# Optimization experiments

Measured on AMD Instinct MI355X. Metric: run time of the kernel, lower is better.

The kernel has to match this reference:

```python
import jax, jax.numpy as jnp
import numpy as np

NUM_USERS = 50000
NUM_ITEMS = 20000
N_NODES = NUM_USERS + NUM_ITEMS
D = 128
CONTENT_DIM = 512
BATCH = 8192
N_EDGES = 500000
NEG_SLOPE = 0.2  # GATConv leaky_relu slope


def setup_inputs() -> dict:
    key = jax.random.key(0)
    ks = jax.random.split(key, 16)
    return {
        "user_ids": jax.random.randint(ks[0], (BATCH,), 0, NUM_USERS),
        "item_ids": jax.random.randint(ks[1], (BATCH,), 0, NUM_ITEMS),
        "content_features": jax.random.normal(ks[2], (BATCH, CONTENT_DIM), jnp.float32),
        "edge_index": jax.random.randint(ks[3], (2, N_EDGES), 0, N_NODES),
        "user_emb_w": jax.random.normal(ks[4], (NUM_USERS, D), jnp.float32) * 0.05,
        "item_emb_w": jax.random.normal(ks[5], (NUM_ITEMS, D), jnp.float32) * 0.05,
        "content_proj_w": jax.random.normal(ks[6], (D, CONTENT_DIM), jnp.float32) * 0.04,
        "content_proj_b": jnp.zeros((D,), jnp.float32),
        "conv1_lin_w": jax.random.normal(ks[7], (2 * D, 2 * D), jnp.float32) * 0.06,
        "conv1_att_src": jax.random.normal(ks[8], (2, D), jnp.float32) * 0.1,
        "conv1_att_dst": jax.random.normal(ks[9], (2, D), jnp.float32) * 0.1,
        "conv1_bias": jnp.zeros((2 * D,), jnp.float32),
        "conv2_lin_w": jax.random.normal(ks[10], (D, 2 * D), jnp.float32) * 0.06,
        "conv2_att_src": jax.random.normal(ks[11], (1, D), jnp.float32) * 0.1,
        "conv2_att_dst": jax.random.normal(ks[12], (1, D), jnp.float32) * 0.1,
        "conv2_bias": jnp.zeros((D,), jnp.float32),
        "pred_w1": jax.random.normal(ks[13], (D, 3 * D), jnp.float32) * 0.05,
        "pred_b1": jnp.zeros((D,), jnp.float32),
        "pred_w2": jax.random.normal(ks[14], (1, D), jnp.float32) * 0.09,
        "pred_b2": jnp.zeros((1,), jnp.float32),
    }


def gat_conv(x, src, dst, lin_w, att_src, att_dst, bias, heads, out_ch):
    # PyG GATConv (shared lin for src/dst, concat=True, add_self_loops handled outside)
    n = x.shape[0]
    h = (x @ lin_w.T).reshape(n, heads, out_ch)          # [N,H,C]
    a_src = jnp.sum(h * att_src, axis=-1)                # [N,H]
    a_dst = jnp.sum(h * att_dst, axis=-1)                # [N,H]
    alpha = jax.nn.leaky_relu(a_src[src] + a_dst[dst], NEG_SLOPE)  # [E,H]
    # softmax over incoming edges of each destination node
    amax = jax.ops.segment_max(alpha, dst, num_segments=n)
    ex = jnp.exp(alpha - amax[dst])
    denom = jax.ops.segment_sum(ex, dst, num_segments=n)
    w = ex / denom[dst]                                  # [E,H]
    out = jax.ops.segment_sum(h[src] * w[:, :, None], dst, num_segments=n)
    return out.reshape(n, heads * out_ch) + bias


def _forward(user_ids, item_ids, edge_index, content_features, user_emb_w, item_emb_w,
             content_proj_w, content_proj_b, conv1_lin_w, conv1_att_src, conv1_att_dst,
             conv1_bias, conv2_lin_w, conv2_att_src, conv2_att_dst, conv2_bias,
             pred_w1, pred_b1, pred_w2, pred_b2):
    u_emb = user_emb_w[user_ids]                         # [B,D]
    i_emb = item_emb_w[item_ids]                         # [B,D]
    c_emb = content_features @ content_proj_w.T + content_proj_b  # [B,D]
    # scatter-init sparse node features (only batch nodes are nonzero, as in source)
    x = jnp.zeros((N_NODES, 2 * D), jnp.float32)
    x = x.at[user_ids].set(jnp.concatenate([u_emb, jnp.zeros_like(c_emb)], axis=1))
    x = x.at[NUM_USERS + item_ids].set(jnp.concatenate([i_emb, c_emb], axis=1))
    # add self loops (fill_value irrelevant: edge_weight unused by GATConv)
    loops = jnp.arange(N_NODES, dtype=edge_index.dtype)
    src = jnp.concatenate([edge_index[0], loops])
    dst = jnp.concatenate([edge_index[1], loops])
    x = jax.nn.elu(gat_conv(x, src, dst, conv1_lin_w, conv1_att_src, conv1_att_dst, conv1_bias, 2, D))
    # dropout inactive (eval mode)
    x = gat_conv(x, src, dst, conv2_lin_w, conv2_att_src, conv2_att_dst, conv2_bias, 1, D)
    combined = jnp.concatenate([u_emb, x[NUM_USERS + item_ids], x[user_ids]], axis=1)  # [B,3D]
    h = jax.nn.relu(combined @ pred_w1.T + pred_b1)
    return (h @ pred_w2.T + pred_b2).squeeze(-1)         # [B]


def reference(user_ids, item_ids, content_features, edge_index, user_emb_w, item_emb_w,
              content_proj_w, content_proj_b, conv1_lin_w, conv1_att_src, conv1_att_dst,
              conv1_bias, conv2_lin_w, conv2_att_src, conv2_att_dst, conv2_bias,
              pred_w1, pred_b1, pred_w2, pred_b2):
    return _forward(user_ids, item_ids, edge_index, content_features, user_emb_w, item_emb_w,
                    content_proj_w, content_proj_b, conv1_lin_w, conv1_att_src, conv1_att_dst,
                    conv1_bias, conv2_lin_w, conv2_att_src, conv2_att_dst, conv2_bias,
                    pred_w1, pred_b1, pred_w2, pred_b2)
```

## Files before the change

### kernel.cpp

```cpp
#include <hip/hip_runtime.h>
#include <hip/hip_bf16.h>

#define NU 50000
#define NI 20000
#define NN 70000
#define DD 128
#define BB 8192
#define EE 500000
#define ET 570000
#define NTASK 16384

__device__ __forceinline__ float lrelu(float x) { return x > 0.f ? x : 0.2f * x; }

typedef __attribute__((ext_vector_type(8))) short bf16x8;
typedef __attribute__((ext_vector_type(8))) unsigned short u16x8;
typedef __attribute__((ext_vector_type(4))) float f32x4;

__device__ __forceinline__ unsigned short f2bf_rne(float f) {
  unsigned int u = __builtin_bit_cast(unsigned int, f);
  u += 0x7FFFu + ((u >> 16) & 1u);
  return (unsigned short)(u >> 16);
}
__device__ __forceinline__ float bf2f(unsigned short h) {
  unsigned int u = ((unsigned int)h) << 16;
  return __builtin_bit_cast(float, u);
}

template <int GATHER>
__global__ __launch_bounds__(256) void gemm_mfma(
    const float* __restrict__ A,
    const unsigned short* __restrict__ Bh, const unsigned short* __restrict__ Bl,
    const float* __restrict__ bias, float* __restrict__ C, int ldc,
    int M, int N, int K, int act,
    const int* __restrict__ idx0, const int* __restrict__ idx1,
    const int* __restrict__ mapv,
    const float* __restrict__ gA0, const float* __restrict__ gA1) {
  __shared__ __align__(16) unsigned short sAh[8][64][8];
  __shared__ __align__(16) unsigned short sAl[8][64][8];
  __shared__ __align__(16) unsigned short sBh[8][64][8];
  __shared__ __align__(16) unsigned short sBl[8][64][8];
  int tid = threadIdx.x;
  int bm = blockIdx.x * 64, bn = blockIdx.y * 64;
  int lane = tid & 63, w = tid >> 6;
  int wr = (w >> 1) * 32, wc = (w & 1) * 32;
  int fr = lane & 15, fk = lane >> 4;
  f32x4 acc[2][2] = {};

  for (int k0 = 0; k0 < K; k0 += 64) {
    __syncthreads();
#pragma unroll
    for (int t = 0; t < 2; t++) {
      int f = tid + t * 256;
      int row = f >> 3, kb = f & 7;
      int kg = k0 + kb * 8;
      const float* ap;
      if (GATHER == 1) {
        int sec = kg >> 7;
        int kc = kg & 127;
        int r = bm + row;
        if (sec == 0)      ap = &gA0[(size_t)idx0[r] * 128 + kc];
        else if (sec == 1) ap = &gA1[(size_t)mapv[NU + idx1[r]] * 128 + kc];
        else               ap = &gA1[(size_t)mapv[idx0[r]] * 128 + kc];
      } else if (GATHER == 2) {
        ap = &gA0[(size_t)idx0[bm + row] * K + kg];
      } else {
        ap = &A[(size_t)(bm + row) * K + kg];
      }
      float4 v0 = *reinterpret_cast<const float4*>(ap);
      float4 v1 = *reinterpret_cast<const float4*>(ap + 4);
      float vv[8] = {v0.x, v0.y, v0.z, v0.w, v1.x, v1.y, v1.z, v1.w};
      u16x8 hv, lv;
#pragma unroll
      for (int j = 0; j < 8; j++) {
        unsigned short hh = f2bf_rne(vv[j]);
        hv[j] = hh;
        lv[j] = (unsigned short)(__builtin_bit_cast(unsigned int, vv[j] - bf2f(hh)) >> 16);
      }
      *reinterpret_cast<u16x8*>(&sAh[kb][row][0]) = hv;
      *reinterpret_cast<u16x8*>(&sAl[kb][row][0]) = lv;
    }
#pragma unroll
    for (int t = 0; t < 2; t++) {
      int f = tid + t * 256;
      int row = f >> 3, kb = f & 7;
      int kg = k0 + kb * 8;
      *reinterpret_cast<u16x8*>(&sBh[kb][row][0]) =
          *reinterpret_cast<const u16x8*>(&Bh[(size_t)(bn + row) * K + kg]);
      *reinterpret_cast<u16x8*>(&sBl[kb][row][0]) =
          *reinterpret_cast<const u16x8*>(&Bl[(size_t)(bn + row) * K + kg]);
    }
    __syncthreads();
#pragma unroll
    for (int s = 0; s < 2; s++) {
      int kb = s * 4 + fk;
      bf16x8 ah0 = *reinterpret_cast<const bf16x8*>(&sAh[kb][wr + fr][0]);
      bf16x8 ah1 = *reinterpret_cast<const bf16x8*>(&sAh[kb][wr + 16 + fr][0]);
      bf16x8 al0 = *reinterpret_cast<const bf16x8*>(&sAl[kb][wr + fr][0]);
      bf16x8 al1 = *reinterpret_cast<const bf16x8*>(&sAl[kb][wr + 16 + fr][0]);
      bf16x8 bh0 = *reinterpret_cast<const bf16x8*>(&sBh[kb][wc + fr][0]);
      bf16x8 bh1 = *reinterpret_cast<const bf16x8*>(&sBh[kb][wc + 16 + fr][0]);
      bf16x8 bl0 = *reinterpret_cast<const bf16x8*>(&sBl[kb][wc + fr][0]);
      bf16x8 bl1 = *reinterpret_cast<const bf16x8*>(&sBl[kb][wc + 16 + fr][0]);
      acc[0][0] = __builtin_amdgcn_mfma_f32_16x16x32_bf16(al0, bh0, acc[0][0], 0, 0, 0);
      acc[0][0] = __builtin_amdgcn_mfma_f32_16x16x32_bf16(ah0, bl0, acc[0][0], 0, 0, 0);
      acc[0][0] = __builtin_amdgcn_mfma_f32_16x16x32_bf16(ah0, bh0, acc[0][0], 0, 0, 0);
      acc[0][1] = __builtin_amdgcn_mfma_f32_16x16x32_bf16(al0, bh1, acc[0][1], 0, 0, 0);
      acc[0][1] = __builtin_amdgcn_mfma_f32_16x16x32_bf16(ah0, bl1, acc[0][1], 0, 0, 0);
      acc[0][1] = __builtin_amdgcn_mfma_f32_16x16x32_bf16(ah0, bh1, acc[0][1], 0, 0, 0);
      acc[1][0] = __builtin_amdgcn_mfma_f32_16x16x32_bf16(al1, bh0, acc[1][0], 0, 0, 0);
      acc[1][0] = __builtin_amdgcn_mfma_f32_16x16x32_bf16(ah1, bl0, acc[1][0], 0, 0, 0);
      acc[1][0] = __builtin_amdgcn_mfma_f32_16x16x32_bf16(ah1, bh0, acc[1][0], 0, 0, 0);
      acc[1][1] = __builtin_amdgcn_mfma_f32_16x16x32_bf16(al1, bh1, acc[1][1], 0, 0, 0);
      acc[1][1] = __builtin_amdgcn_mfma_f32_16x16x32_bf16(ah1, bl1, acc[1][1], 0, 0, 0);
      acc[1][1] = __builtin_amdgcn_mfma_f32_16x16x32_bf16(ah1, bh1, acc[1][1], 0, 0, 0);
    }
  }
#pragma unroll
  for (int j = 0; j < 2; j++) {
    int col = bn + wc + j * 16 + fr;
    float bj = bias ? bias[col] : 0.f;
#pragma unroll
    for (int i = 0; i < 2; i++) {
#pragma unroll
      for (int r = 0; r < 4; r++) {
        int row = bm + wr + i * 16 + fk * 4 + r;
        float v = acc[i][j][r] + bj;
        if (act == 1) v = fmaxf(v, 0.f);
        C[(size_t)row * ldc + col] = v;
      }
    }
  }
}

#define EB 2227
#define SPLB 832
#define XAB 4096
__global__ __launch_bounds__(256) void setup_kernel(
    const int* __restrict__ ei, const int* __restrict__ uid, const int* __restrict__ iid,
    int* __restrict__ deg, int* __restrict__ winner,
    const float* __restrict__ wc, unsigned short* wch, unsigned short* wcl,
    const float* __restrict__ w1, unsigned short* w1h, unsigned short* w1l,
    const float* __restrict__ w2, unsigned short* w2h, unsigned short* w2l,
    const float* __restrict__ pw1, unsigned short* p1h, unsigned short* p1l,
    const float* __restrict__ uemb, const float* __restrict__ iemb,
    float* __restrict__ Xa, int* __restrict__ map) {
  int bid = blockIdx.x, tid = threadIdx.x;
  if (bid < EB) {
    int e = bid * 256 + tid;
    if (e < BB) atomicMax(&winner[iid[e]], e);
    if (e >= ET) return;
    int dst = (e < EE) ? ei[EE + e] : (e - EE);
    atomicAdd(&deg[dst], 1);
    return;
  }
  if (bid < EB + SPLB) {
    int i = (bid - EB) * 256 + tid;
    const float* w; unsigned short* h; unsigned short* l; int idx;
    if (i < 65536) { w = wc; h = wch; l = wcl; idx = i; }
    else if (i < 131072) { w = w1; h = w1h; l = w1l; idx = i - 65536; }
    else if (i < 163840) { w = w2; h = w2h; l = w2l; idx = i - 131072; }
    else { w = pw1; h = p1h; l = p1l; idx = i - 163840; }
    float f = w[idx];
    unsigned short hh = f2bf_rne(f);
    h[idx] = hh;
    l[idx] = (unsigned short)(__builtin_bit_cast(unsigned int, f - bf2f(hh)) >> 16);
    return;
  }
  int t = (bid - EB - SPLB) * 4 + (tid >> 6);
  int lane = tid & 63;
  int c4 = lane * 4;
  if (t < BB) {
    int u = uid[t];
    float4 v = make_float4(0.f, 0.f, 0.f, 0.f);
    if (c4 < DD) v = *reinterpret_cast<const float4*>(&uemb[(size_t)u * DD + c4]);
    *reinterpret_cast<float4*>(&Xa[(size_t)t * 256 + c4]) = v;
    if (lane == 0) map[u] = t;
  } else {
    int it = iid[t - BB];
    if (c4 < DD) {
      float4 v = *reinterpret_cast<const float4*>(&iemb[(size_t)it * DD + c4]);
      *reinterpret_cast<float4*>(&Xa[(size_t)t * 256 + c4]) = v;
    }
    if (lane == 0) map[NU + it] = t;
  }
}

__global__ void rowstart_kernel(const int* __restrict__ deg, const int* __restrict__ winner,
                                const int* __restrict__ iid,
                                int* __restrict__ rowstart, int* __restrict__ fill,
                                int* __restrict__ counter, int* __restrict__ widx) {
  int v = blockIdx.x * 256 + threadIdx.x;
  if (v < BB) widx[v] = winner[iid[v]];
  if (v >= NN) return;
  int s = atomicAdd(counter, deg[v]);
  rowstart[v] = s;
  fill[v] = s;
}

__global__ void fill_mark_kernel(const int* __restrict__ ei, int* __restrict__ fill,
                                 int* __restrict__ col, const int* __restrict__ map,
                                 unsigned char* __restrict__ needed) {
  int e = blockIdx.x * 256 + threadIdx.x;
  if (e >= ET) return;
  int src, dst;
  if (e < EE) { src = ei[e]; dst = ei[EE + e]; }
  else { src = e - EE; dst = src; }
  int pos = atomicAdd(&fill[dst], 1);
  col[pos] = src;
  if (map[dst] >= 0) needed[src] = 1;
}

__global__ __launch_bounds__(256) void a1q_kernel(
    const int* __restrict__ uid, const int* __restrict__ iid,
    const float* __restrict__ Ha,
    const float* __restrict__ atts, const float* __restrict__ attd,
    const float* __restrict__ w2,
    const float* __restrict__ att2s, const float* __restrict__ att2d,
    float* __restrict__ a1s, float* __restrict__ a1d,
    float* __restrict__ qs, float* __restrict__ qd) {
  int t = blockIdx.x * 4 + (threadIdx.x >> 6);
  int lane = threadIdx.x & 63;
  if (t >= NTASK) {
    int k = (t - NTASK) * 64 + lane;
    float s = 0.f, d = 0.f;
#pragma unroll 4
    for (int j = 0; j < DD; j++) {
      float w = w2[(size_t)j * 256 + k];
      s += att2s[j] * w;
      d += att2d[j] * w;
    }
    qs[k] = s;
    qd[k] = d;
    return;
  }
  int v = (t < BB) ? uid[t] : NU + iid[t - BB];
  int head = lane >> 5, c = (lane & 31) * 4;
  float4 hv = *reinterpret_cast<const float4*>(&Ha[(size_t)t * 256 + head * DD + c]);
  float4 sv = *reinterpret_cast<const float4*>(&atts[head * DD + c]);
  float4 dv = *reinterpret_cast<const float4*>(&attd[head * DD + c]);
  float ps = hv.x * sv.x + hv.y * sv.y + hv.z * sv.z + hv.w * sv.w;
  float pd = hv.x * dv.x + hv.y * dv.y + hv.z * dv.z + hv.w * dv.w;
  for (int o = 1; o < 32; o <<= 1) { ps += __shfl_xor(ps, o); pd += __shfl_xor(pd, o); }
  if ((lane & 31) == 0) {
    a1s[(size_t)v * 2 + head] = ps;
    a1d[(size_t)v * 2 + head] = pd;
  }
}

__global__ __launch_bounds__(256) void conv1_agg_kernel(
    const int* __restrict__ col, const int* __restrict__ rowstart,
    const int* __restrict__ deg, const float* __restrict__ Ha,
    const int* __restrict__ map, const unsigned char* __restrict__ needed,
    const float* __restrict__ a1s, const float* __restrict__ a1d,
    const float* __restrict__ bias,
    const float* __restrict__ qs, const float* __restrict__ qd,
    unsigned short* __restrict__ x1b, float* __restrict__ a2s, float* __restrict__ a2d) {
  int v = blockIdx.x * 4 + (threadIdx.x >> 6);
  int lane = threadIdx.x & 63;
  if (!needed[v]) return;
  int head = lane >> 5;
  int d = deg[v], s0 = rowstart[v];
  float2 adv = *reinterpret_cast<const float2*>(&a1d[(size_t)v * 2]);
  float4 acc = make_float4(0.f, 0.f, 0.f, 0.f);
  float den;
  if (d <= 64) {
    bool act = lane < d;
    int ci = act ? col[s0 + lane] : 0;
    float2 asv = make_float2(0.f, 0.f);
    int ri = -1;
    if (act) {
      asv = *reinterpret_cast<const float2*>(&a1s[(size_t)ci * 2]);
      ri = map[ci];
    }
    float al0 = act ? lrelu(asv.x + adv.x) : -1e30f;
    float al1 = act ? lrelu(asv.y + adv.y) : -1e30f;
    float m0 = al0, m1 = al1;
#pragma unroll
    for (int o = 1; o < 64; o <<= 1) {
      m0 = fmaxf(m0, __shfl_xor(m0, o));
      m1 = fmaxf(m1, __shfl_xor(m1, o));
    }
    float ex0 = act ? __expf(al0 - m0) : 0.f;
    float ex1 = act ? __expf(al1 - m1) : 0.f;
    float cs0 = ex0, cs1 = ex1;
#pragma unroll
    for (int o = 1; o < 64; o <<= 1) {
      cs0 += __shfl_xor(cs0, o);
      cs1 += __shfl_xor(cs1, o);
    }
    den = head ? cs1 : cs0;
    for (int i2 = 0; i2 < d; i2++) {
      int r = __shfl(ri, i2);
      if (r >= 0) {
        float e0 = __shfl(ex0, i2), e1 = __shfl(ex1, i2);
        float ex = head ? e1 : e0;
        float4 hv = *reinterpret_cast<const float4*>(&Ha[((size_t)r << 8) + (lane << 2)]);
        acc.x += ex * hv.x; acc.y += ex * hv.y; acc.z += ex * hv.z; acc.w += ex * hv.w;
      }
    }
  } else {
    float m0 = -1e30f, m1 = -1e30f, den0 = 0.f, den1 = 0.f;
    for (int c0 = 0; c0 < d; c0 += 64) {
      int i = c0 + lane;
      bool act = i < d;
      int ci = act ? col[s0 + i] : 0;
      float2 asv = make_float2(0.f, 0.f);
      int ri = -1;
      if (act) {
        asv = *reinterpret_cast<const float2*>(&a1s[(size_t)ci * 2]);
        ri = map[ci];
      }
      float al0 = act ? lrelu(asv.x + adv.x) : -1e30f;
      float al1 = act ? lrelu(asv.y + adv.y) : -1e30f;
      float cm0 = al0, cm1 = al1;
#pragma unroll
      for (int o = 1; o < 64; o <<= 1) {
        cm0 = fmaxf(cm0, __shfl_xor(cm0, o));
        cm1 = fmaxf(cm1, __shfl_xor(cm1, o));
      }
      float nm0 = fmaxf(m0, cm0), nm1 = fmaxf(m1, cm1);
      float ex0 = act ? __expf(al0 - nm0) : 0.f;
      float ex1 = act ? __expf(al1 - nm1) : 0.f;
      float s0f = __expf(m0 - nm0), s1f = __expf(m1 - nm1);
      float cs0 = ex0, cs1 = ex1;
#pragma unroll
      for (int o = 1; o < 64; o <<= 1) {
        cs0 += __shfl_xor(cs0, o);
        cs1 += __shfl_xor(cs1, o);
      }
      den0 = den0 * s0f + cs0;
      den1 = den1 * s1f + cs1;
      float sc = head ? s1f : s0f;
      acc.x *= sc; acc.y *= sc; acc.z *= sc; acc.w *= sc;
      int n = min(64, d - c0);
      for (int i2 = 0; i2 < n; i2++) {
        int r = __shfl(ri, i2);
        if (r >= 0) {
          float e0 = __shfl(ex0, i2), e1 = __shfl(ex1, i2);
          float ex = head ? e1 : e0;
          float4 hv = *reinterpret_cast<const float4*>(&Ha[((size_t)r << 8) + (lane << 2)]);
          acc.x += ex * hv.x; acc.y += ex * hv.y; acc.z += ex * hv.z; acc.w += ex * hv.w;
        }
      }
      m0 = nm0; m1 = nm1;
    }
    den = head ? den1 : den0;
  }
  float inv = 1.f / den;
  float4 b4 = *reinterpret_cast<const float4*>(&bias[lane << 2]);
  float4 o;
  o.x = fmaf(acc.x, inv, b4.x);
  o.y = fmaf(acc.y, inv, b4.y);
  o.z = fmaf(acc.z, inv, b4.z);
  o.w = fmaf(acc.w, inv, b4.w);
  o.x = o.x > 0.f ? o.x : __expf(o.x) - 1.f;
  o.y = o.y > 0.f ? o.y : __expf(o.y) - 1.f;
  o.z = o.z > 0.f ? o.z : __expf(o.z) - 1.f;
  o.w = o.w > 0.f ? o.w : __expf(o.w) - 1.f;
  ushort4 st;
  st.x = f2bf_rne(o.x); st.y = f2bf_rne(o.y);
  st.z = f2bf_rne(o.z); st.w = f2bf_rne(o.w);
  *reinterpret_cast<ushort4*>(&x1b[((size_t)v << 8) + (lane << 2)]) = st;
  float4 sv = *reinterpret_cast<const float4*>(&qs[lane << 2]);
  float4 dv = *reinterpret_cast<const float4*>(&qd[lane << 2]);
  float ps = o.x * sv.x + o.y * sv.y + o.z * sv.z + o.w * sv.w;
  float pd = o.x * dv.x + o.y * dv.y + o.z * dv.z + o.w * dv.w;
#pragma unroll
  for (int of = 1; of < 64; of <<= 1) { ps += __shfl_xor(ps, of); pd += __shfl_xor(pd, of); }
  if (lane == 0) { a2s[v] = ps; a2d[v] = pd; }
}

__global__ __launch_bounds__(256) void conv2_agg_kernel(
    const int* __restrict__ uid, const int* __restrict__ iid,
    const int* __restrict__ col, const int* __restrict__ rowstart,
    const int* __restrict__ deg, const int* __restrict__ map,
    const unsigned short* __restrict__ x1b,
    const float* __restrict__ a2s, const float* __restrict__ a2d,
    float* __restrict__ agg) {
  int t = blockIdx.x * 4 + (threadIdx.x >> 6);
  int lane = threadIdx.x & 63;
  int v = (t < BB) ? uid[t] : NU + iid[t - BB];
  if (map[v] != t) return;
  int d = deg[v], s0 = rowstart[v];
  float ad = a2d[v];
  float4 acc = make_float4(0.f, 0.f, 0.f, 0.f);
  float den;
  if (d <= 64) {
    bool act = lane < d;
    int ci = act ? col[s0 + lane] : 0;
    float as = act ? a2s[ci] : 0.f;
    float al = act ? lrelu(as + ad) : -1e30f;
    float m = al;
#pragma unroll
    for (int o = 1; o < 64; o <<= 1) m = fmaxf(m, __shfl_xor(m, o));
    float ex = act ? __expf(al - m) : 0.f;
    float cs = ex;
#pragma unroll
    for (int o = 1; o < 64; o <<= 1) cs += __shfl_xor(cs, o);
    den = cs;
    for (int i2 = 0; i2 < d; i2++) {
      int r = __shfl(ci, i2);
      float e = __shfl(ex, i2);
      ushort4 hv = *reinterpret_cast<const ushort4*>(&x1b[((size_t)r << 8) + (lane << 2)]);
      acc.x += e * bf2f(hv.x); acc.y += e * bf2f(hv.y);
      acc.z += e * bf2f(hv.z); acc.w += e * bf2f(hv.w);
    }
  } else {
    float m = -1e30f; den = 0.f;
    for (int c0 = 0; c0 < d; c0 += 64) {
      int i = c0 + lane;
      bool act = i < d;
      int ci = act ? col[s0 + i] : 0;
      float as = act ? a2s[ci] : 0.f;
      float al = act ? lrelu(as + ad) : -1e30f;
      float cm = al;
#pragma unroll
      for (int o = 1; o < 64; o <<= 1) cm = fmaxf(cm, __shfl_xor(cm, o));
      float nm = fmaxf(m, cm);
      float ex = act ? __expf(al - nm) : 0.f;
      float sf = __expf(m - nm);
      float cs = ex;
#pragma unroll
      for (int o = 1; o < 64; o <<= 1) cs += __shfl_xor(cs, o);
      den = den * sf + cs;
      acc.x *= sf; acc.y *= sf; acc.z *= sf; acc.w *= sf;
      int n = min(64, d - c0);
      for (int i2 = 0; i2 < n; i2++) {
        int r = __shfl(ci, i2);
        float e = __shfl(ex, i2);
        ushort4 hv = *reinterpret_cast<const ushort4*>(&x1b[((size_t)r << 8) + (lane << 2)]);
        acc.x += e * bf2f(hv.x); acc.y += e * bf2f(hv.y);
        acc.z += e * bf2f(hv.z); acc.w += e * bf2f(hv.w);
      }
      m = nm;
    }
  }
  float inv = 1.f / den;
  float4 o = make_float4(acc.x * inv, acc.y * inv, acc.z * inv, acc.w * inv);
  *reinterpret_cast<float4*>(&agg[((size_t)t << 8) + (lane << 2)]) = o;
}

__global__ __launch_bounds__(256) void final_kernel(
    const float* __restrict__ ph, const float* __restrict__ w2,
    const float* __restrict__ b2, float* __restrict__ out) {
  int b = blockIdx.x * 4 + (threadIdx.x >> 6);
  int lane = threadIdx.x & 63;
  float2 hv = *reinterpret_cast<const float2*>(&ph[((size_t)b << 7) + (lane << 1)]);
  float2 wv = *reinterpret_cast<const float2*>(&w2[lane << 1]);
  float s = hv.x * wv.x + hv.y * wv.y;
  for (int o = 1; o < 64; o <<= 1) s += __shfl_xor(s, o);
  if (lane == 0) out[b] = s + b2[0];
}

extern "C" void kernel_launch(void* const* d_in, const int* in_sizes, int n_in,
                              void* d_out, int out_size, void* d_ws, size_t ws_size,
                              hipStream_t stream) {
  const int* uid = (const int*)d_in[0];
  const int* iid = (const int*)d_in[1];
  const float* content = (const float*)d_in[2];
  const int* ei = (const int*)d_in[3];
  const float* uemb = (const float*)d_in[4];
  const float* iemb = (const float*)d_in[5];
  const float* wc = (const float*)d_in[6];
  const float* bc = (const float*)d_in[7];
  const float* w1 = (const float*)d_in[8];
  const float* att1s = (const float*)d_in[9];
  const float* att1d = (const float*)d_in[10];
  const float* b1 = (const float*)d_in[11];
  const float* w2 = (const float*)d_in[12];
  const float* att2s = (const float*)d_in[13];
  const float* att2d = (const float*)d_in[14];
  const float* b2c = (const float*)d_in[15];
  const float* pw1 = (const float*)d_in[16];
  const float* pb1 = (const float*)d_in[17];
  const float* pw2 = (const float*)d_in[18];
  const float* pb2 = (const float*)d_in[19];
  float* out = (float*)d_out;
  char* ws = (char*)d_ws;

  size_t off = 0;
  auto alloc = [&](size_t bytes) {
    size_t o = off;
    off += (bytes + 255) & ~(size_t)255;
    return o;
  };
  size_t o_winner  = alloc(NI * 4);
  size_t o_map     = alloc(NN * 4);
  size_t o_a1s     = alloc((size_t)NN * 2 * 4);
  size_t o_a1d     = alloc((size_t)NN * 2 * 4);
  size_t o_deg     = alloc(NN * 4);
  size_t o_rs      = alloc(NN * 4);
  size_t o_fill    = alloc(NN * 4);
  size_t o_cnt     = alloc(4);
  size_t o_needed  = alloc(NN);
  size_t o_col     = alloc((size_t)ET * 4);
  size_t o_a2s     = alloc(NN * 4);
  size_t o_a2d     = alloc(NN * 4);
  size_t o_qs      = alloc(256 * 4);
  size_t o_qd      = alloc(256 * 4);
  size_t o_widx    = alloc(BB * 4);
  size_t o_wch = alloc(65536 * 2),  o_wcl = alloc(65536 * 2);
  size_t o_w1h = alloc(65536 * 2),  o_w1l = alloc(65536 * 2);
  size_t o_w2h = alloc(32768 * 2),  o_w2l = alloc(32768 * 2);
  size_t o_p1h = alloc(49152 * 2),  o_p1l = alloc(49152 * 2);
  size_t o_r1    = alloc(16777216 + 16777216);
  size_t o_xa    = o_r1;
  size_t o_ha    = o_r1 + 16777216;
  size_t o_agg   = o_r1;
  size_t o_out2c = o_r1 + 16777216;
  size_t o_ph    = o_r1;
  size_t o_x1b   = alloc((size_t)NN * 256 * 2);
  (void)ws_size; (void)in_sizes; (void)n_in; (void)out_size;

  int*   winner = (int*)(ws + o_winner);
  int*   map    = (int*)(ws + o_map);
  float* a1s    = (float*)(ws + o_a1s);
  float* a1d    = (float*)(ws + o_a1d);
  int*   deg    = (int*)(ws + o_deg);
  int*   rs     = (int*)(ws + o_rs);
  int*   fill   = (int*)(ws + o_fill);
  int*   cnt    = (int*)(ws + o_cnt);
  unsigned char* needed = (unsigned char*)(ws + o_needed);
  int*   col    = (int*)(ws + o_col);
  float* a2s    = (float*)(ws + o_a2s);
  float* a2d    = (float*)(ws + o_a2d);
  float* qs     = (float*)(ws + o_qs);
  float* qd     = (float*)(ws + o_qd);
  int*   widx   = (int*)(ws + o_widx);
  unsigned short* wch = (unsigned short*)(ws + o_wch);
  unsigned short* wcl = (unsigned short*)(ws + o_wcl);
  unsigned short* w1h = (unsigned short*)(ws + o_w1h);
  unsigned short* w1l = (unsigned short*)(ws + o_w1l);
  unsigned short* w2h = (unsigned short*)(ws + o_w2h);
  unsigned short* w2l = (unsigned short*)(ws + o_w2l);
  unsigned short* p1h = (unsigned short*)(ws + o_p1h);
  unsigned short* p1l = (unsigned short*)(ws + o_p1l);
  float* Xa     = (float*)(ws + o_xa);
  float* Ha     = (float*)(ws + o_ha);
  float* agg    = (float*)(ws + o_agg);
  float* out2c  = (float*)(ws + o_out2c);
  float* ph     = (float*)(ws + o_ph);
  unsigned short* x1b = (unsigned short*)(ws + o_x1b);

  hipMemsetAsync(ws + o_winner, 0xFF, o_map - o_winner + (size_t)NN * 4, stream);
  hipMemsetAsync(ws + o_a1s, 0, o_a1d - o_a1s + (size_t)NN * 2 * 4, stream);
  hipMemsetAsync(ws + o_deg, 0, o_needed - o_deg + NN, stream);

  setup_kernel<<<EB + SPLB + XAB, 256, 0, stream>>>(
      ei, uid, iid, deg, winner,
      wc, wch, wcl, w1, w1h, w1l, w2, w2h, w2l, pw1, p1h, p1l,
      uemb, iemb, Xa, map);
  rowstart_kernel<<<(NN + 255) / 256, 256, 0, stream>>>(deg, winner, iid, rs, fill, cnt, widx);
  {
    dim3 g(BB / 64, DD / 64);
    gemm_mfma<2><<<g, 256, 0, stream>>>(nullptr, wch, wcl, bc, Xa + (size_t)BB * 256 + 128,
                                        256, BB, DD, 512, 0,
                                        widx, nullptr, nullptr, content, nullptr);
  }
  fill_mark_kernel<<<(ET + 255) / 256, 256, 0, stream>>>(ei, fill, col, map, needed);
  {
    dim3 g(NTASK / 64, 256 / 64);
    gemm_mfma<0><<<g, 256, 0, stream>>>(Xa, w1h, w1l, nullptr, Ha, 256, NTASK, 256, 256, 0,
                                        nullptr, nullptr, nullptr, nullptr, nullptr);
  }
  a1q_kernel<<<NTASK / 4 + 1, 256, 0, stream>>>(uid, iid, Ha, att1s, att1d,
                                                w2, att2s, att2d, a1s, a1d, qs, qd);
  conv1_agg_kernel<<<NN / 4, 256, 0, stream>>>(col, rs, deg, Ha, map, needed,
                                               a1s, a1d, b1, qs, qd, x1b, a2s, a2d);
  conv2_agg_kernel<<<NTASK / 4, 256, 0, stream>>>(uid, iid, col, rs, deg, map,
                                                  x1b, a2s, a2d, agg);
  {
    dim3 g(NTASK / 64, DD / 64);
    gemm_mfma<0><<<g, 256, 0, stream>>>(agg, w2h, w2l, b2c, out2c, 128, NTASK, DD, 256, 0,
                                        nullptr, nullptr, nullptr, nullptr, nullptr);
  }
  {
    dim3 g(BB / 64, DD / 64);
    gemm_mfma<1><<<g, 256, 0, stream>>>(nullptr, p1h, p1l, pb1, ph, 128, BB, DD, 384, 1,
                                        uid, iid, map, uemb, out2c);
  }
  final_kernel<<<BB / 4, 256, 0, stream>>>(ph, pw2, pb2, out);
}
```

Baseline: 224.2 us.

## Fuse attention-logit dot products into conv1 GEMM epilogue and store H in bf16

Removes the separate a1q kernel. The conv1 linear GEMM now computes the per-head attention source/destination dot products in its epilogue through lane shuffles and atomic adds, and writes its output as bf16 instead of fp32. The att2 projection vectors (qs/qd) move into an extra block of the rowstart kernel. This cuts one launch and one full read of H, and halves the gather traffic for H in the conv1 aggregation. In exchange it adds atomics to a1s/a1d, which now rely on the earlier zero memset, and it loses precision on the aggregated features.

```diff
diff --git a/kernel.cpp b/kernel.cpp
--- a/kernel.cpp
+++ b/kernel.cpp
@@ -26,15 +26,18 @@
   return __builtin_bit_cast(float, u);
 }
 
-template <int GATHER>
+template <int GATHER, int MODE>
 __global__ __launch_bounds__(256) void gemm_mfma(
     const float* __restrict__ A,
     const unsigned short* __restrict__ Bh, const unsigned short* __restrict__ Bl,
-    const float* __restrict__ bias, float* __restrict__ C, int ldc,
+    const float* __restrict__ bias, float* __restrict__ C,
+    unsigned short* __restrict__ Cb, int ldc,
     int M, int N, int K, int act,
     const int* __restrict__ idx0, const int* __restrict__ idx1,
     const int* __restrict__ mapv,
-    const float* __restrict__ gA0, const float* __restrict__ gA1) {
+    const float* __restrict__ gA0, const float* __restrict__ gA1,
+    const float* __restrict__ att_s, const float* __restrict__ att_d,
+    float* __restrict__ a1s, float* __restrict__ a1d) {
   __shared__ __align__(16) unsigned short sAh[8][64][8];
   __shared__ __align__(16) unsigned short sAl[8][64][8];
   __shared__ __align__(16) unsigned short sBh[8][64][8];
@@ -115,6 +118,50 @@
       acc[1][1] = __builtin_amdgcn_mfma_f32_16x16x32_bf16(ah1, bh1, acc[1][1], 0, 0, 0);
     }
   }
+  if (MODE == 1) {
+    int head = bn >> 7;
+    float ps[2][4] = {{0.f}}, pd[2][4] = {{0.f}};
+#pragma unroll
+    for (int j = 0; j < 2; j++) {
+      int col = bn + wc + j * 16 + fr;
+      float asc = att_s[col], adc = att_d[col];
+#pragma unroll
+      for (int i = 0; i < 2; i++) {
+#pragma unroll
+        for (int r = 0; r < 4; r++) {
+          float v = acc[i][j][r];
+          ps[i][r] += v * asc;
+          pd[i][r] += v * adc;
+          Cb[(size_t)(bm + wr + i * 16 + fk * 4 + r) * ldc + col] = f2bf_rne(v);
+        }
+      }
+    }
+#pragma unroll
+    for (int o = 1; o < 16; o <<= 1) {
+#pragma unroll
+      for (int i = 0; i < 2; i++)
+#pragma unroll
+        for (int r = 0; r < 4; r++) {
+          ps[i][r] += __shfl_xor(ps[i][r], o);
+          pd[i][r] += __shfl_xor(pd[i][r], o);
+        }
+    }
+    if (fr == 0) {
+#pragma unroll
+      for (int i = 0; i < 2; i++) {
+#pragma unroll
+        for (int r = 0; r < 4; r++) {
+          int t = bm + wr + i * 16 + fk * 4 + r;
+          int v = (t < BB) ? idx0[t] : NU + idx1[t - BB];
+          if (mapv[v] == t) {
+            atomicAdd(&a1s[(size_t)v * 2 + head], ps[i][r]);
+            atomicAdd(&a1d[(size_t)v * 2 + head], pd[i][r]);
+          }
+        }
+      }
+    }
+    return;
+  }
 #pragma unroll
   for (int j = 0; j < 2; j++) {
     int col = bn + wc + j * 16 + fr;
@@ -188,8 +235,25 @@
 __global__ void rowstart_kernel(const int* __restrict__ deg, const int* __restrict__ winner,
                                 const int* __restrict__ iid,
                                 int* __restrict__ rowstart, int* __restrict__ fill,
-                                int* __restrict__ counter, int* __restrict__ widx) {
-  int v = blockIdx.x * 256 + threadIdx.x;
+                                int* __restrict__ counter, int* __restrict__ widx,
+                                const float* __restrict__ w2,
+                                const float* __restrict__ att2s, const float* __restrict__ att2d,
+                                float* __restrict__ qs, float* __restrict__ qd) {
+  int blk = blockIdx.x;
+  if (blk == (NN + 255) / 256) {
+    int k = threadIdx.x;
+    float s = 0.f, d = 0.f;
+#pragma unroll 4
+    for (int j = 0; j < DD; j++) {
+      float w = w2[(size_t)j * 256 + k];
+      s += att2s[j] * w;
+      d += att2d[j] * w;
+    }
+    qs[k] = s;
+    qd[k] = d;
+    return;
+  }
+  int v = blk * 256 + threadIdx.x;
   if (v < BB) widx[v] = winner[iid[v]];
   if (v >= NN) return;
   int s = atomicAdd(counter, deg[v]);
@@ -210,46 +274,9 @@
   if (map[dst] >= 0) needed[src] = 1;
 }
 
-__global__ __launch_bounds__(256) void a1q_kernel(
-    const int* __restrict__ uid, const int* __restrict__ iid,
-    const float* __restrict__ Ha,
-    const float* __restrict__ atts, const float* __restrict__ attd,
-    const float* __restrict__ w2,
-    const float* __restrict__ att2s, const float* __restrict__ att2d,
-    float* __restrict__ a1s, float* __restrict__ a1d,
-    float* __restrict__ qs, float* __restrict__ qd) {
-  int t = blockIdx.x * 4 + (threadIdx.x >> 6);
-  int lane = threadIdx.x & 63;
-  if (t >= NTASK) {
-    int k = (t - NTASK) * 64 + lane;
-    float s = 0.f, d = 0.f;
-#pragma unroll 4
-    for (int j = 0; j < DD; j++) {
-      float w = w2[(size_t)j * 256 + k];
-      s += att2s[j] * w;
-      d += att2d[j] * w;
-    }
-    qs[k] = s;
-    qd[k] = d;
-    return;
-  }
-  int v = (t < BB) ? uid[t] : NU + iid[t - BB];
-  int head = lane >> 5, c = (lane & 31) * 4;
-  float4 hv = *reinterpret_cast<const float4*>(&Ha[(size_t)t * 256 + head * DD + c]);
-  float4 sv = *reinterpret_cast<const float4*>(&atts[head * DD + c]);
-  float4 dv = *reinterpret_cast<const float4*>(&attd[head * DD + c]);
-  float ps = hv.x * sv.x + hv.y * sv.y + hv.z * sv.z + hv.w * sv.w;
-  float pd = hv.x * dv.x + hv.y * dv.y + hv.z * dv.z + hv.w * dv.w;
-  for (int o = 1; o < 32; o <<= 1) { ps += __shfl_xor(ps, o); pd += __shfl_xor(pd, o); }
-  if ((lane & 31) == 0) {
-    a1s[(size_t)v * 2 + head] = ps;
-    a1d[(size_t)v * 2 + head] = pd;
-  }
-}
-
 __global__ __launch_bounds__(256) void conv1_agg_kernel(
     const int* __restrict__ col, const int* __restrict__ rowstart,
-    const int* __restrict__ deg, const float* __restrict__ Ha,
+    const int* __restrict__ deg, const unsigned short* __restrict__ Hb,
     const int* __restrict__ map, const unsigned char* __restrict__ needed,
     const float* __restrict__ a1s, const float* __restrict__ a1d,
     const float* __restrict__ bias,
@@ -294,8 +321,9 @@
       if (r >= 0) {
         float e0 = __shfl(ex0, i2), e1 = __shfl(ex1, i2);
         float ex = head ? e1 : e0;
-        float4 hv = *reinterpret_cast<const float4*>(&Ha[((size_t)r << 8) + (lane << 2)]);
-        acc.x += ex * hv.x; acc.y += ex * hv.y; acc.z += ex * hv.z; acc.w += ex * hv.w;
+        ushort4 hv = *reinterpret_cast<const ushort4*>(&Hb[((size_t)r << 8) + (lane << 2)]);
+        acc.x += ex * bf2f(hv.x); acc.y += ex * bf2f(hv.y);
+        acc.z += ex * bf2f(hv.z); acc.w += ex * bf2f(hv.w);
       }
     }
   } else {
@@ -338,8 +366,9 @@
         if (r >= 0) {
           float e0 = __shfl(ex0, i2), e1 = __shfl(ex1, i2);
           float ex = head ? e1 : e0;
-          float4 hv = *reinterpret_cast<const float4*>(&Ha[((size_t)r << 8) + (lane << 2)]);
-          acc.x += ex * hv.x; acc.y += ex * hv.y; acc.z += ex * hv.z; acc.w += ex * hv.w;
+          ushort4 hv = *reinterpret_cast<const ushort4*>(&Hb[((size_t)r << 8) + (lane << 2)]);
+          acc.x += ex * bf2f(hv.x); acc.y += ex * bf2f(hv.y);
+          acc.z += ex * bf2f(hv.z); acc.w += ex * bf2f(hv.w);
         }
       }
       m0 = nm0; m1 = nm1;
@@ -503,9 +532,9 @@
   size_t o_w1h = alloc(65536 * 2),  o_w1l = alloc(65536 * 2);
   size_t o_w2h = alloc(32768 * 2),  o_w2l = alloc(32768 * 2);
   size_t o_p1h = alloc(49152 * 2),  o_p1l = alloc(49152 * 2);
-  size_t o_r1    = alloc(16777216 + 16777216);
+  size_t o_r1    = alloc(16777216 + 8388608);
   size_t o_xa    = o_r1;
-  size_t o_ha    = o_r1 + 16777216;
+  size_t o_hb    = o_r1 + 16777216;
   size_t o_agg   = o_r1;
   size_t o_out2c = o_r1 + 16777216;
   size_t o_ph    = o_r1;
@@ -536,7 +565,7 @@
   unsigned short* p1h = (unsigned short*)(ws + o_p1h);
   unsigned short* p1l = (unsigned short*)(ws + o_p1l);
   float* Xa     = (float*)(ws + o_xa);
-  float* Ha     = (float*)(ws + o_ha);
+  unsigned short* Hb = (unsigned short*)(ws + o_hb);
   float* agg    = (float*)(ws + o_agg);
   float* out2c  = (float*)(ws + o_out2c);
   float* ph     = (float*)(ws + o_ph);
@@ -550,34 +579,40 @@
       ei, uid, iid, deg, winner,
       wc, wch, wcl, w1, w1h, w1l, w2, w2h, w2l, pw1, p1h, p1l,
       uemb, iemb, Xa, map);
-  rowstart_kernel<<<(NN + 255) / 256, 256, 0, stream>>>(deg, winner, iid, rs, fill, cnt, widx);
+  rowstart_kernel<<<(NN + 255) / 256 + 1, 256, 0, stream>>>(
+      deg, winner, iid, rs, fill, cnt, widx, w2, att2s, att2d, qs, qd);
   {
     dim3 g(BB / 64, DD / 64);
-    gemm_mfma<2><<<g, 256, 0, stream>>>(nullptr, wch, wcl, bc, Xa + (size_t)BB * 256 + 128,
-                                        256, BB, DD, 512, 0,
-                                        widx, nullptr, nullptr, content, nullptr);
+    gemm_mfma<2, 0><<<g, 256, 0, stream>>>(
+        nullptr, wch, wcl, bc, Xa + (size_t)BB * 256 + 128, nullptr, 256,
+        BB, DD, 512, 0, widx, nullptr, nullptr, content, nullptr,
+        nullptr, nullptr, nullptr, nullptr);
   }
   fill_mark_kernel<<<(ET + 255) / 256, 256, 0, stream>>>(ei, fill, col, map, needed);
   {
     dim3 g(NTASK / 64, 256 / 64);
-    gemm_mfma<0><<<g, 256, 0, stream>>>(Xa, w1h, w1l, nullptr, Ha, 256, NTASK, 256, 256, 0,
-                                        nullptr, nullptr, nullptr, nullptr, nullptr);
-  }
-  a1q_kernel<<<NTASK / 4 + 1, 256, 0, stream>>>(uid, iid, Ha, att1s, att1d,
-                                                w2, att2s, att2d, a1s, a1d, qs, qd);
-  conv1_agg_kernel<<<NN / 4, 256, 0, stream>>>(col, rs, deg, Ha, map, needed,
+    gemm_mfma<0, 1><<<g, 256, 0, stream>>>(
+        Xa, w1h, w1l, nullptr, nullptr, Hb, 256,
+        NTASK, 256, 256, 0, uid, iid, map, nullptr, nullptr,
+        att1s, att1d, a1s, a1d);
+  }
+  conv1_agg_kernel<<<NN / 4, 256, 0, stream>>>(col, rs, deg, Hb, map, needed,
                                                a1s, a1d, b1, qs, qd, x1b, a2s, a2d);
   conv2_agg_kernel<<<NTASK / 4, 256, 0, stream>>>(uid, iid, col, rs, deg, map,
                                                   x1b, a2s, a2d, agg);
   {
     dim3 g(NTASK / 64, DD / 64);
-    gemm_mfma<0><<<g, 256, 0, stream>>>(agg, w2h, w2l, b2c, out2c, 128, NTASK, DD, 256, 0,
-                                        nullptr, nullptr, nullptr, nullptr, nullptr);
+    gemm_mfma<0, 0><<<g, 256, 0, stream>>>(
+        agg, w2h, w2l, b2c, out2c, nullptr, 128,
+        NTASK, DD, 256, 0, nullptr, nullptr, nullptr, nullptr, nullptr,
+        nullptr, nullptr, nullptr, nullptr);
   }
   {
     dim3 g(BB / 64, DD / 64);
-    gemm_mfma<1><<<g, 256, 0, stream>>>(nullptr, p1h, p1l, pb1, ph, 128, BB, DD, 384, 1,
-                                        uid, iid, map, uemb, out2c);
+    gemm_mfma<1, 0><<<g, 256, 0, stream>>>(
+        nullptr, p1h, p1l, pb1, ph, nullptr, 128,
+        BB, DD, 384, 1, uid, iid, map, uemb, out2c,
+        nullptr, nullptr, nullptr, nullptr);
   }
   final_kernel<<<BB / 4, 256, 0, stream>>>(ph, pw2, pb2, out);
 }
```

After: 220.5 us. Within noise of the previous version (-1.6%).
